# Performance work log

Measured on AMD Instinct MI355X. Metric: run time of the kernel, lower is better.

## Reference

```python
import jax, jax.numpy as jnp
import numpy as np

H, NH, NKV, HD, S, B = 4096, 32, 8, 128, 2048, 1
QMAX = 127.0  # int8 symmetric


def fake_quant(x, axis=None):
    """Symmetric int8 fake quantization with straight-through estimator.
    axis=None -> per-tensor dynamic scale; axis=int -> per-channel along that axis."""
    if axis is None:
        amax = jnp.max(jnp.abs(x))
    else:
        amax = jnp.max(jnp.abs(x), axis=axis, keepdims=True)
    scale = jnp.maximum(amax, 1e-8) / QMAX
    q = jnp.clip(jnp.round(x / scale), -QMAX - 1, QMAX) * scale
    return x + jax.lax.stop_gradient(q - x)


def quant_linear(x, w):
    # weight: per-output-channel quant (reduce over in-features axis=1);
    # activation: per-tensor dynamic quant
    xq = fake_quant(x)
    wq = fake_quant(w, axis=1)
    return jnp.einsum('bsh,oh->bso', xq, wq)


def rotate_half(x):
    x1, x2 = jnp.split(x, 2, axis=-1)
    return jnp.concatenate([-x2, x1], axis=-1)


def apply_rope(q, k, cos, sin):
    # q: [B,NH,S,HD], k: [B,NKV,S,HD], cos/sin: [B,S,HD]
    cos = cos[:, None, :, :]
    sin = sin[:, None, :, :]
    return q * cos + rotate_half(q) * sin, k * cos + rotate_half(k) * sin


def setup_inputs() -> dict:
    key = jax.random.key(0)
    ks = jax.random.split(key, 6)
    hidden_states = jax.random.normal(ks[0], (B, S, H), jnp.float32)
    # additive causal mask
    neg = jnp.finfo(jnp.float32).min
    mask = jnp.where(jnp.tril(jnp.ones((S, S), bool)), 0.0, neg)
    attention_mask = jnp.broadcast_to(mask, (B, 1, S, S)).astype(jnp.float32)
    # rotary cos/sin
    inv_freq = 1.0 / (10000.0 ** (jnp.arange(0, HD, 2, dtype=jnp.float32) / HD))
    t = jnp.arange(S, dtype=jnp.float32)
    freqs = jnp.outer(t, inv_freq)                     # [S, HD/2]
    emb = jnp.concatenate([freqs, freqs], axis=-1)     # [S, HD]
    cos = jnp.broadcast_to(jnp.cos(emb), (B, S, HD))
    sin = jnp.broadcast_to(jnp.sin(emb), (B, S, HD))
    sc = 0.02
    wq = jax.random.normal(ks[1], (H, H), jnp.float32) * sc
    wk = jax.random.normal(ks[2], (NKV * HD, H), jnp.float32) * sc
    wv = jax.random.normal(ks[3], (NKV * HD, H), jnp.float32) * sc
    wo = jax.random.normal(ks[4], (H, H), jnp.float32) * sc
    return {"hidden_states": hidden_states, "attention_mask": attention_mask,
            "cos": cos, "sin": sin, "wq": wq, "wk": wk, "wv": wv, "wo": wo}


def reference(hidden_states, attention_mask, cos, sin, wq, wk, wv, wo):
    b, s, _ = hidden_states.shape
    scaling = HD ** -0.5
    q = quant_linear(hidden_states, wq).reshape(b, s, NH, HD).transpose(0, 2, 1, 3)
    k = quant_linear(hidden_states, wk).reshape(b, s, NKV, HD).transpose(0, 2, 1, 3)
    v = quant_linear(hidden_states, wv).reshape(b, s, NKV, HD).transpose(0, 2, 1, 3)
    q, k = apply_rope(q, k, cos, sin)
    groups = NH // NKV
    k = jnp.repeat(k, groups, axis=1)  # [B,NH,S,HD]
    v = jnp.repeat(v, groups, axis=1)
    # quantize before QK^T
    qq = fake_quant(q)
    kq = fake_quant(k)
    attn = jnp.einsum('bhqd,bhkd->bhqk', qq, kq) * scaling
    attn = attn + attention_mask
    attn = jnp.maximum(attn, jnp.finfo(attn.dtype).min)
    attn = jax.nn.softmax(attn.astype(jnp.float32), axis=-1).astype(q.dtype)
    # quantize before PV
    pq = fake_quant(attn)
    vq = fake_quant(v)
    out = jnp.einsum('bhqk,bhkd->bhqd', pq, vq)
    out = out.transpose(0, 2, 1, 3).reshape(b, s, NH * HD)
    out = quant_linear(out, wo)
    return out
```

## Files before the change

### kernel.cpp

```cpp
#include <hip/hip_runtime.h>
#include <cstdint>
#include <cstddef>


#define S_LEN   2048
#define HDIM    4096
#define NHEADS  32
#define NKVH    8
#define HEADD   128
#define QMAXF   127.0f
#define ROPE_BLOCKS 20480

typedef _Float16 half8  __attribute__((ext_vector_type(8)));
typedef float    floatx4 __attribute__((ext_vector_type(4)));

__device__ __forceinline__ float wave_max64(float v){
#pragma unroll
  for (int off = 32; off > 0; off >>= 1) v = fmaxf(v, __shfl_xor(v, off));
  return v;
}
__device__ __forceinline__ float grp16_max(float v){
#pragma unroll
  for (int off = 8; off > 0; off >>= 1) v = fmaxf(v, __shfl_xor(v, off));
  return v;
}
__device__ __forceinline__ float grp16_sum(float v){
#pragma unroll
  for (int off = 8; off > 0; off >>= 1) v += __shfl_xor(v, off);
  return v;
}
__device__ __forceinline__ void atomic_max_f(unsigned* p, float v){
  atomicMax(p, __float_as_uint(v));
}
__device__ __forceinline__ float q8(float x, float scale){
  return fminf(fmaxf(rintf(x / scale), -128.f), 127.f);
}
__device__ __forceinline__ void gload_lds16(const _Float16* g, _Float16* l){
  __builtin_amdgcn_global_load_lds((const __attribute__((address_space(1))) void*)g,
                                   (__attribute__((address_space(3))) void*)l, 16, 0, 0);
}

__device__ __forceinline__ void block_atomic_max(float m, unsigned* out){
  m = wave_max64(m);
  __shared__ float red[4];
  int wid = threadIdx.x >> 6;
  if ((threadIdx.x & 63) == 0) red[wid] = m;
  __syncthreads();
  if (threadIdx.x == 0)
    atomic_max_f(out, fmaxf(fmaxf(red[0], red[1]), fmaxf(red[2], red[3])));
}

__global__ void k_init(float* scal){ if (threadIdx.x < 16) scal[threadIdx.x] = 0.0f; }

__global__ void k_amax(const float* __restrict__ x, size_t n4, unsigned* __restrict__ out){
  size_t i = (size_t)blockIdx.x * blockDim.x + threadIdx.x;
  size_t stride = (size_t)gridDim.x * blockDim.x;
  float m = 0.f;
  for (; i < n4; i += stride){
    float4 v = ((const float4*)x)[i];
    m = fmaxf(m, fmaxf(fmaxf(fabsf(v.x), fabsf(v.y)), fmaxf(fabsf(v.z), fabsf(v.w))));
  }
  block_atomic_max(m, out);
}

__global__ void k_amax_v(const float* __restrict__ Y, unsigned* __restrict__ out){
  size_t i = (size_t)blockIdx.x * blockDim.x + threadIdx.x;
  size_t stride = (size_t)gridDim.x * blockDim.x;
  float m = 0.f;
  for (size_t e = i; e < (size_t)S_LEN * 1024; e += stride){
    size_t s = e >> 10; int c = (int)(e & 1023);
    m = fmaxf(m, fabsf(Y[s * 6144 + 5120 + c]));
  }
  block_atomic_max(m, out);
}

__global__ void k_quant(const float* __restrict__ x, _Float16* __restrict__ q,
                        size_t n4, const float* __restrict__ amax){
  float scale = fmaxf(*amax, 1e-8f) / QMAXF;
  size_t i = (size_t)blockIdx.x * blockDim.x + threadIdx.x;
  size_t stride = (size_t)gridDim.x * blockDim.x;
  for (; i < n4; i += stride){
    float4 v = ((const float4*)x)[i];
    union { _Float16 h[4]; uint2 u; } pk;
    pk.h[0] = (_Float16)q8(v.x, scale);
    pk.h[1] = (_Float16)q8(v.y, scale);
    pk.h[2] = (_Float16)q8(v.z, scale);
    pk.h[3] = (_Float16)q8(v.w, scale);
    ((uint2*)q)[i] = pk.u;
  }
}

__global__ __launch_bounds__(256) void k_quant_w(
    const float* __restrict__ wq, const float* __restrict__ wk,
    const float* __restrict__ wv, const float* __restrict__ wo,
    _Float16* __restrict__ Wall, _Float16* __restrict__ Wo,
    float* __restrict__ wsc)
{
  int row = blockIdx.x;
  const float* src; _Float16* dst;
  if (row < 4096)      { src = wq + (size_t)row * HDIM;          dst = Wall + (size_t)row * HDIM; }
  else if (row < 5120) { src = wk + (size_t)(row - 4096) * HDIM; dst = Wall + (size_t)row * HDIM; }
  else if (row < 6144) { src = wv + (size_t)(row - 5120) * HDIM; dst = Wall + (size_t)row * HDIM; }
  else                 { src = wo + (size_t)(row - 6144) * HDIM; dst = Wo + (size_t)(row - 6144) * HDIM; }
  float4 v[4]; float m = 0.f;
#pragma unroll
  for (int i = 0; i < 4; i++){
    v[i] = ((const float4*)src)[threadIdx.x + i * 256];
    m = fmaxf(m, fmaxf(fmaxf(fabsf(v[i].x), fabsf(v[i].y)), fmaxf(fabsf(v[i].z), fabsf(v[i].w))));
  }
  m = wave_max64(m);
  __shared__ float red[4];
  int wid = threadIdx.x >> 6;
  if ((threadIdx.x & 63) == 0) red[wid] = m;
  __syncthreads();
  float am = fmaxf(fmaxf(red[0], red[1]), fmaxf(red[2], red[3]));
  float scale = fmaxf(am, 1e-8f) / QMAXF;
  if (threadIdx.x == 0) wsc[row] = scale;
#pragma unroll
  for (int i = 0; i < 4; i++){
    union { _Float16 h[4]; uint2 u; } pk;
    pk.h[0] = (_Float16)q8(v[i].x, scale);
    pk.h[1] = (_Float16)q8(v[i].y, scale);
    pk.h[2] = (_Float16)q8(v[i].z, scale);
    pk.h[3] = (_Float16)q8(v[i].w, scale);
    ((uint2*)dst)[threadIdx.x + i * 256] = pk.u;
  }
}

__global__ __launch_bounds__(256) void k_rope(
    float* __restrict__ Y, const float* __restrict__ cosb,
    const float* __restrict__ sinb,
    float* __restrict__ qpart, float* __restrict__ kpart)
{
  int idx = blockIdx.x * 256 + threadIdx.x;
  int s = idx / (40 * 64);
  int rem = idx - s * 40 * 64;
  int head = rem >> 6;
  int d = rem & 63;
  size_t base = (size_t)s * 6144 + (head < 32 ? head * 128 : 4096 + (head - 32) * 128);
  float x1 = Y[base + d], x2 = Y[base + d + 64];
  float c1 = cosb[s * 128 + d],      s1 = sinb[s * 128 + d];
  float c2 = cosb[s * 128 + d + 64], s2 = sinb[s * 128 + d + 64];
  float o1 = x1 * c1 - x2 * s1;
  float o2 = x2 * c2 + x1 * s2;
  Y[base + d] = o1; Y[base + d + 64] = o2;
  float m = wave_max64(fmaxf(fabsf(o1), fabsf(o2)));
  __shared__ float wmax[4]; __shared__ int wisq[4];
  int wid = threadIdx.x >> 6;
  if ((threadIdx.x & 63) == 0){ wmax[wid] = m; wisq[wid] = (head < 32); }
  __syncthreads();
  if (threadIdx.x == 0){
    float qm = 0.f, km = 0.f;
#pragma unroll
    for (int w = 0; w < 4; w++){
      if (wisq[w]) qm = fmaxf(qm, wmax[w]); else km = fmaxf(km, wmax[w]);
    }
    qpart[blockIdx.x] = qm; kpart[blockIdx.x] = km;
  }
}

__global__ __launch_bounds__(256) void k_reduce_qk(
    const float* __restrict__ qpart, const float* __restrict__ kpart,
    float* __restrict__ scal)
{
  const float* src = blockIdx.x ? kpart : qpart;
  float m = 0.f;
  for (int i = threadIdx.x; i < ROPE_BLOCKS; i += 256) m = fmaxf(m, src[i]);
  m = wave_max64(m);
  __shared__ float red[4];
  int wid = threadIdx.x >> 6;
  if ((threadIdx.x & 63) == 0) red[wid] = m;
  __syncthreads();
  if (threadIdx.x == 0)
    scal[1 + blockIdx.x] = fmaxf(fmaxf(red[0], red[1]), fmaxf(red[2], red[3]));
}

__global__ __launch_bounds__(256) void k_quant_qk(
    const float* __restrict__ Y, _Float16* __restrict__ Qh,
    _Float16* __restrict__ Kh, const float* __restrict__ scal)
{
  int i = blockIdx.x * 256 + threadIdx.x;
  int s = i / 1280, c4 = i - s * 1280;
  int col = c4 * 4;
  float4 v = *(const float4*)(Y + (size_t)s * 6144 + col);
  float scale = fmaxf(col < 4096 ? scal[1] : scal[2], 1e-8f) / QMAXF;
  union { _Float16 h[4]; uint2 u; } pk;
  pk.h[0] = (_Float16)q8(v.x, scale);
  pk.h[1] = (_Float16)q8(v.y, scale);
  pk.h[2] = (_Float16)q8(v.z, scale);
  pk.h[3] = (_Float16)q8(v.w, scale);
  if (col < 4096) *(uint2*)(Qh + (size_t)s * 4096 + col) = pk.u;
  else            *(uint2*)(Kh + (size_t)s * 1024 + (col - 4096)) = pk.u;
}

__global__ __launch_bounds__(256) void k_quant_vt(
    const float* __restrict__ Y, _Float16* __restrict__ Vt,
    const float* __restrict__ scal)
{
  __shared__ _Float16 sT[64][72];
  const int s0 = blockIdx.x * 64, kvh = blockIdx.y, dh = blockIdx.z;
  const float scale = fmaxf(scal[3], 1e-8f) / QMAXF;
  const int d = threadIdx.x & 63, srow = threadIdx.x >> 6;
#pragma unroll
  for (int i = 0; i < 16; i++){
    int s = srow + i * 4;
    float v = Y[(size_t)(s0 + s) * 6144 + 5120 + kvh * 128 + dh * 64 + d];
    sT[d][s] = (_Float16)q8(v, scale);
  }
  __syncthreads();
  const int dr = threadIdx.x >> 2, j = threadIdx.x & 3;
  _Float16* dst = Vt + (size_t)kvh * HEADD * S_LEN + (size_t)(dh * 64 + dr) * S_LEN + s0 + j * 16;
  *(uint4*)(dst)     = *(const uint4*)(&sT[dr][j * 16]);
  *(uint4*)(dst + 8) = *(const uint4*)(&sT[dr][j * 16 + 8]);
}

__global__ __launch_bounds__(256) void k_gemm_nt(
    const _Float16* __restrict__ A, const _Float16* __restrict__ B,
    const float* __restrict__ amax_a, const float* __restrict__ sb,
    float* __restrict__ C, int M, int N, int K)
{
  __shared__ _Float16 sA[128 * 32];
  __shared__ _Float16 sB[128 * 32];
  const int m0 = blockIdx.x * 128;
  const int n0 = blockIdx.y * 128;
  const int tid = threadIdx.x;
  const int w = tid >> 6, lane = tid & 63;
  const int quad = lane >> 4, l16 = lane & 15;
  const int wm = (w & 1) * 64, wn = (w >> 1) * 64;
  floatx4 acc[4][4] = {};
  const int srow = w * 16 + (lane >> 2);
  const int scol = (lane & 3) * 8;
  const _Float16* gA0 = A + (size_t)(m0 + srow) * K + scol;
  const _Float16* gA1 = A + (size_t)(m0 + 64 + srow) * K + scol;
  const _Float16* gB0 = B + (size_t)(n0 + srow) * K + scol;
  const _Float16* gB1 = B + (size_t)(n0 + 64 + srow) * K + scol;
  _Float16* dA0 = sA + w * 512 + lane * 8;
  _Float16* dA1 = sA + 2048 + w * 512 + lane * 8;
  _Float16* dB0 = sB + w * 512 + lane * 8;
  _Float16* dB1 = sB + 2048 + w * 512 + lane * 8;

  for (int k0 = 0; k0 < K; k0 += 32){
    __syncthreads();
    gload_lds16(gA0 + k0, dA0);
    gload_lds16(gA1 + k0, dA1);
    gload_lds16(gB0 + k0, dB0);
    gload_lds16(gB1 + k0, dB1);
    __syncthreads();
    half8 af[4], bf[4];
#pragma unroll
    for (int i = 0; i < 4; i++){
      af[i] = *(const half8*)(sA + (wm + i * 16 + l16) * 32 + quad * 8);
      bf[i] = *(const half8*)(sB + (wn + i * 16 + l16) * 32 + quad * 8);
    }
#pragma unroll
    for (int i = 0; i < 4; i++)
#pragma unroll
      for (int j = 0; j < 4; j++)
        acc[i][j] = __builtin_amdgcn_mfma_f32_16x16x32_f16(af[i], bf[j], acc[i][j], 0, 0, 0);
  }
  const float sa = fmaxf(*amax_a, 1e-8f) / QMAXF;
#pragma unroll
  for (int i = 0; i < 4; i++){
    int row = m0 + wm + i * 16 + quad * 4;
#pragma unroll
    for (int j = 0; j < 4; j++){
      int col = n0 + wn + j * 16 + l16;
      float sc2 = sa * sb[col];
#pragma unroll
      for (int rr = 0; rr < 4; rr++)
        C[(size_t)(row + rr) * N + col] = acc[i][j][rr] * sc2;
    }
  }
}

__global__ __launch_bounds__(256, 4) void k_attn(
    const _Float16* __restrict__ Qh,
    const _Float16* __restrict__ Kh,
    const _Float16* __restrict__ Vt,
    const float* __restrict__ scal,
    float* __restrict__ AO)
{
  const int jj = blockIdx.y >> 3;
  const int aa = (jj & 2) ? (int)((blockIdx.x + 16) & 31) : (int)blockIdx.x;
  const int qb = (jj & 1) ? (31 - aa) : aa;
  const int h   = blockIdx.y;
  const int kvh = h >> 2;
  const int tid = threadIdx.x;
  const int wid = tid >> 6, lane = tid & 63;
  const int quad = lane >> 4, l16 = lane & 15;

  __shared__ _Float16 sKV[2][8192];
  __shared__ _Float16 sP[4][1024];

  const float s_q = fmaxf(scal[1], 1e-8f) / QMAXF;
  const float s_k = fmaxf(scal[2], 1e-8f) / QMAXF;
  const float s_v = fmaxf(scal[3], 1e-8f) / QMAXF;
  const float qkscale = s_q * s_k * 0.08838834764831845f;
  const float osc = s_v * (1.0f / QMAXF);

  const int r   = tid >> 2, seg = tid & 3;
  int kst[4];
#pragma unroll
  for (int i = 0; i < 4; i++){
    int c = seg * 4 + i;
    kst[i] = r * 128 + ((c & 8) | ((c ^ (r & 7)) & 7)) * 8;
  }
  const int vr = tid >> 1, vh = tid & 1;
  int vst[4];
#pragma unroll
  for (int i = 0; i < 4; i++){
    int c = vh * 4 + i;
    vst[i] = vr * 64 + ((c ^ (vr & 7)) & 7) * 8;
  }
  int krd[4];
#pragma unroll
  for (int kk = 0; kk < 4; kk++){
    int c = kk * 4 + quad;
    krd[kk] = l16 * 128 + ((c & 8) | ((c ^ (l16 & 7)) & 7)) * 8;
  }
  const int vrd0 = l16 * 64 + ((quad       ^ (l16 & 7)) & 7) * 8;
  const int vrd1 = l16 * 64 + (((quad ^ 4) ^ (l16 & 7)) & 7) * 8;

  const _Float16* gK0 = Kh + (size_t)r * 1024 + (size_t)kvh * 128 + seg * 32;
  const _Float16* gV0 = Vt + (size_t)kvh * (HEADD * S_LEN) + (size_t)vr * S_LEN + vh * 32;

  const int qrow = qb * 64 + wid * 16 + l16;
  half8 qf[4];
#pragma unroll
  for (int kk = 0; kk < 4; kk++)
    qf[kk] = *(const half8*)(Qh + (size_t)qrow * 4096 + h * 128 + kk * 32 + quad * 8);
  const int q_of_reg = qb * 64 + wid * 16 + quad * 4;

  float mrow[4], lrow[4];
#pragma unroll
  for (int rr = 0; rr < 4; rr++){ mrow[rr] = -__builtin_inff(); lrow[rr] = 0.f; }

  {
    const uint4* g = (const uint4*)gK0;
    uint4 t0 = g[0], t1 = g[1], t2 = g[2], t3 = g[3];
    _Float16* b = sKV[0];
    *(uint4*)(b + kst[0]) = t0; *(uint4*)(b + kst[1]) = t1;
    *(uint4*)(b + kst[2]) = t2; *(uint4*)(b + kst[3]) = t3;
  }
  __syncthreads();

  for (int kt = 0; kt <= qb; ++kt){
    uint4 t0, t1, t2, t3;
    if (kt < qb){
      const uint4* g = (const uint4*)(gK0 + (size_t)(kt + 1) * 65536);
      t0 = g[0]; t1 = g[1]; t2 = g[2]; t3 = g[3];
    }
    const _Float16* kb = sKV[kt & 1];
    float sv[4][4];
    const bool diag = (kt == qb);
    __builtin_amdgcn_s_setprio(1);
#pragma unroll
    for (int nt = 0; nt < 4; nt++){
      floatx4 c = {};
#pragma unroll
      for (int kk = 0; kk < 4; kk++){
        half8 bf = *(const half8*)(kb + nt * 2048 + krd[kk]);
        c = __builtin_amdgcn_mfma_f32_16x16x32_f16(qf[kk], bf, c, 0, 0, 0);
      }
      if (diag){
        int kpos = kt * 64 + nt * 16 + l16;
#pragma unroll
        for (int rr = 0; rr < 4; rr++)
          sv[nt][rr] = (kpos <= q_of_reg + rr) ? c[rr] * qkscale : -__builtin_inff();
      } else {
#pragma unroll
        for (int rr = 0; rr < 4; rr++) sv[nt][rr] = c[rr] * qkscale;
      }
    }
    __builtin_amdgcn_s_setprio(0);
    if (kt < qb){
      _Float16* b = sKV[(kt + 1) & 1];
      *(uint4*)(b + kst[0]) = t0; *(uint4*)(b + kst[1]) = t1;
      *(uint4*)(b + kst[2]) = t2; *(uint4*)(b + kst[3]) = t3;
    }
#pragma unroll
    for (int rr = 0; rr < 4; rr++){
      float lmax = fmaxf(fmaxf(sv[0][rr], sv[1][rr]), fmaxf(sv[2][rr], sv[3][rr]));
      float tmax = grp16_max(lmax);
      float mnew = fmaxf(mrow[rr], tmax);
      float lsum = 0.f;
#pragma unroll
      for (int nt = 0; nt < 4; nt++) lsum += __expf(sv[nt][rr] - mnew);
      lsum = grp16_sum(lsum);
      lrow[rr] = lrow[rr] * __expf(mrow[rr] - mnew) + lsum;
      mrow[rr] = mnew;
    }
    __syncthreads();
  }

  float il[4];
#pragma unroll
  for (int rr = 0; rr < 4; rr++) il[rr] = QMAXF * __builtin_amdgcn_rcpf(lrow[rr]);

  floatx4 accO[8] = {};
  _Float16* sKb = sKV[0];
  _Float16* sVb = sKV[1];
  _Float16* sPw = sP[wid];

  uint4 t0, t1, t2, t3, u0, u1, u2, u3;
  {
    const uint4* g  = (const uint4*)gK0;
    t0 = g[0];  t1 = g[1];  t2 = g[2];  t3 = g[3];
    const uint4* gv = (const uint4*)gV0;
    u0 = gv[0]; u1 = gv[1]; u2 = gv[2]; u3 = gv[3];
  }
  for (int kt = 0; kt <= qb; ++kt){
    __syncthreads();
    *(uint4*)(sKb + kst[0]) = t0; *(uint4*)(sKb + kst[1]) = t1;
    *(uint4*)(sKb + kst[2]) = t2; *(uint4*)(sKb + kst[3]) = t3;
    *(uint4*)(sVb + vst[0]) = u0; *(uint4*)(sVb + vst[1]) = u1;
    *(uint4*)(sVb + vst[2]) = u2; *(uint4*)(sVb + vst[3]) = u3;
    __syncthreads();
    const bool diag = (kt == qb);
    __builtin_amdgcn_s_setprio(1);
#pragma unroll
    for (int nt = 0; nt < 4; nt++){
      floatx4 c = {};
#pragma unroll
      for (int kk = 0; kk < 4; kk++){
        half8 bf = *(const half8*)(sKb + nt * 2048 + krd[kk]);
        c = __builtin_amdgcn_mfma_f32_16x16x32_f16(qf[kk], bf, c, 0, 0, 0);
      }
      int kpos = kt * 64 + nt * 16 + l16;
#pragma unroll
      for (int rr = 0; rr < 4; rr++){
        float pq = fminf(rintf(__expf(c[rr] * qkscale - mrow[rr]) * il[rr]), 127.f);
        if (diag && kpos > q_of_reg + rr) pq = 0.f;
        int row = quad * 4 + rr;
        sPw[row * 64 + ((nt * 2 + (l16 >> 3)) ^ (row & 7)) * 8 + (l16 & 7)] = (_Float16)pq;
      }
    }
    __builtin_amdgcn_s_setprio(0);
    if (kt < qb){
      const uint4* g  = (const uint4*)(gK0 + (size_t)(kt + 1) * 65536);
      t0 = g[0];  t1 = g[1];  t2 = g[2];  t3 = g[3];
      const uint4* gv = (const uint4*)(gV0 + (size_t)(kt + 1) * 64);
      u0 = gv[0]; u1 = gv[1]; u2 = gv[2]; u3 = gv[3];
    }
    half8 pf0 = *(const half8*)(sPw + vrd0);
    half8 pf1 = *(const half8*)(sPw + vrd1);
    __builtin_amdgcn_s_setprio(1);
#pragma unroll
    for (int dt = 0; dt < 8; dt++){
      half8 b0 = *(const half8*)(sVb + dt * 1024 + vrd0);
      half8 b1 = *(const half8*)(sVb + dt * 1024 + vrd1);
      accO[dt] = __builtin_amdgcn_mfma_f32_16x16x32_f16(pf0, b0, accO[dt], 0, 0, 0);
      accO[dt] = __builtin_amdgcn_mfma_f32_16x16x32_f16(pf1, b1, accO[dt], 0, 0, 0);
    }
    __builtin_amdgcn_s_setprio(0);
  }

#pragma unroll
  for (int dt = 0; dt < 8; dt++){
    int col = h * 128 + dt * 16 + l16;
#pragma unroll
    for (int rr = 0; rr < 4; rr++)
      AO[(size_t)(q_of_reg + rr) * 4096 + col] = accO[dt][rr] * osc;
  }
}

extern "C" void kernel_launch(void* const* d_in, const int* in_sizes, int n_in,
                              void* d_out, int out_size, void* d_ws, size_t ws_size,
                              hipStream_t stream)
{
  const float* hidden = (const float*)d_in[0];
  const float* cosb = (const float*)d_in[2];
  const float* sinb = (const float*)d_in[3];
  const float* wq = (const float*)d_in[4];
  const float* wk = (const float*)d_in[5];
  const float* wv = (const float*)d_in[6];
  const float* wo = (const float*)d_in[7];
  float* out = (float*)d_out;

  char* ws = (char*)d_ws;
  size_t off = 0;
  auto alloc = [&](size_t bytes){ size_t o = off; off += (bytes + 255) & ~(size_t)255; return o; };
  float*    scal  = (float*)   (ws + alloc(64));
  float*    wsc   = (float*)   (ws + alloc(10240 * 4));
  float*    qpart = (float*)   (ws + alloc(ROPE_BLOCKS * 4));
  float*    kpart = (float*)   (ws + alloc(ROPE_BLOCKS * 4));
  _Float16* Wall  = (_Float16*)(ws + alloc((size_t)6144 * 4096 * 2));
  _Float16* Wo    = (_Float16*)(ws + alloc((size_t)4096 * 4096 * 2));
  _Float16* Xq    = (_Float16*)(ws + alloc((size_t)2048 * 4096 * 2));
  float*    Y     = (float*)   (ws + alloc((size_t)2048 * 6144 * 4));
  _Float16* Qh  = Xq;
  _Float16* Kh  = Wall;
  _Float16* Vt  = Wall + (size_t)2048 * 1024;
  float*    AO  = Y;
  _Float16* AOq = (_Float16*)((char*)Y + (size_t)2048 * 4096 * 4);

  unsigned* su = (unsigned*)scal;

  k_init<<<dim3(1), dim3(64), 0, stream>>>(scal);
  k_quant_w<<<dim3(10240), dim3(256), 0, stream>>>(wq, wk, wv, wo, Wall, Wo, wsc);
  k_amax<<<dim3(256), dim3(256), 0, stream>>>(hidden, (size_t)(2048 * 4096 / 4), su + 0);
  k_quant<<<dim3(2048), dim3(256), 0, stream>>>(hidden, Xq, (size_t)(2048 * 4096 / 4), scal + 0);
  k_gemm_nt<<<dim3(16, 48), dim3(256), 0, stream>>>(Xq, Wall, scal + 0, wsc, Y, 2048, 6144, 4096);
  k_rope<<<dim3(ROPE_BLOCKS), dim3(256), 0, stream>>>(Y, cosb, sinb, qpart, kpart);
  k_reduce_qk<<<dim3(2), dim3(256), 0, stream>>>(qpart, kpart, scal);
  k_amax_v<<<dim3(256), dim3(256), 0, stream>>>(Y, su + 3);
  k_quant_qk<<<dim3(10240), dim3(256), 0, stream>>>(Y, Qh, Kh, scal);
  k_quant_vt<<<dim3(32, 8, 2), dim3(256), 0, stream>>>(Y, Vt, scal);
  k_attn<<<dim3(32, 32), dim3(256), 0, stream>>>(Qh, Kh, Vt, scal, AO);
  k_amax<<<dim3(256), dim3(256), 0, stream>>>(AO, (size_t)(2048 * 4096 / 4), su + 4);
  k_quant<<<dim3(2048), dim3(256), 0, stream>>>(AO, AOq, (size_t)(2048 * 4096 / 4), scal + 4);
  k_gemm_nt<<<dim3(16, 32), dim3(256), 0, stream>>>(AOq, Wo, scal + 4, wsc + 6144, out, 2048, 4096, 4096);
}
```

Before: 735.5 us.

## Stage attention K/V tiles with direct global-to-LDS loads instead of registers

The attention kernel now copies K and V tiles straight from global memory into LDS through a direct-load helper, in place of loading into registers and then storing to LDS. The XOR swizzle is moved onto the global source addresses so the LDS layout stays the same. This saves registers and LDS store instructions. In the second pass, however, the loads are now issued right before the barrier, so they no longer overlap with the previous tile's compute. The launch-bounds occupancy hint is also lowered from 4 to 2 blocks per CU.

```diff
diff --git a/kernel.cpp b/kernel.cpp
--- a/kernel.cpp
+++ b/kernel.cpp
@@ -273,7 +273,7 @@
   }
 }
 
-__global__ __launch_bounds__(256, 4) void k_attn(
+__global__ __launch_bounds__(256, 2) void k_attn(
     const _Float16* __restrict__ Qh,
     const _Float16* __restrict__ Kh,
     const _Float16* __restrict__ Vt,
@@ -298,20 +298,13 @@
   const float qkscale = s_q * s_k * 0.08838834764831845f;
   const float osc = s_v * (1.0f / QMAXF);
 
-  const int r   = tid >> 2, seg = tid & 3;
-  int kst[4];
-#pragma unroll
-  for (int i = 0; i < 4; i++){
-    int c = seg * 4 + i;
-    kst[i] = r * 128 + ((c & 8) | ((c ^ (r & 7)) & 7)) * 8;
-  }
-  const int vr = tid >> 1, vh = tid & 1;
-  int vst[4];
-#pragma unroll
-  for (int i = 0; i < 4; i++){
-    int c = vh * 4 + i;
-    vst[i] = vr * 64 + ((c ^ (vr & 7)) & 7) * 8;
-  }
+  const int srow7 = (wid * 4 + quad) & 7;
+  const int sch   = (l16 & 8) | ((l16 ^ srow7) & 7);
+  const _Float16* gKs = Kh + (size_t)(wid * 4 + quad) * 1024 + (size_t)kvh * 128 + sch * 8;
+  const int vrg = lane >> 3, vp = lane & 7;
+  const _Float16* gVs = Vt + (size_t)kvh * (HEADD * S_LEN)
+                           + (size_t)(wid * 8 + vrg) * S_LEN + ((vp ^ vrg) & 7) * 8;
+
   int krd[4];
 #pragma unroll
   for (int kk = 0; kk < 4; kk++){
@@ -321,9 +314,6 @@
   const int vrd0 = l16 * 64 + ((quad       ^ (l16 & 7)) & 7) * 8;
   const int vrd1 = l16 * 64 + (((quad ^ 4) ^ (l16 & 7)) & 7) * 8;
 
-  const _Float16* gK0 = Kh + (size_t)r * 1024 + (size_t)kvh * 128 + seg * 32;
-  const _Float16* gV0 = Vt + (size_t)kvh * (HEADD * S_LEN) + (size_t)vr * S_LEN + vh * 32;
-
   const int qrow = qb * 64 + wid * 16 + l16;
   half8 qf[4];
 #pragma unroll
@@ -335,21 +325,28 @@
 #pragma unroll
   for (int rr = 0; rr < 4; rr++){ mrow[rr] = -__builtin_inff(); lrow[rr] = 0.f; }
 
-  {
-    const uint4* g = (const uint4*)gK0;
-    uint4 t0 = g[0], t1 = g[1], t2 = g[2], t3 = g[3];
-    _Float16* b = sKV[0];
-    *(uint4*)(b + kst[0]) = t0; *(uint4*)(b + kst[1]) = t1;
-    *(uint4*)(b + kst[2]) = t2; *(uint4*)(b + kst[3]) = t3;
-  }
+  auto stage_k = [&](int kt, _Float16* buf){
+    const _Float16* g = gKs + (size_t)kt * 65536;
+    _Float16* d = buf + wid * 512;
+    gload_lds16(g,          d);
+    gload_lds16(g + 16384,  d + 2048);
+    gload_lds16(g + 32768,  d + 4096);
+    gload_lds16(g + 49152,  d + 6144);
+  };
+  auto stage_v = [&](int kt, _Float16* buf){
+    const _Float16* g = gVs + (size_t)kt * 64;
+    _Float16* d = buf + wid * 512;
+    gload_lds16(g,          d);
+    gload_lds16(g + 65536,  d + 2048);
+    gload_lds16(g + 131072, d + 4096);
+    gload_lds16(g + 196608, d + 6144);
+  };
+
+  stage_k(0, sKV[0]);
   __syncthreads();
 
   for (int kt = 0; kt <= qb; ++kt){
-    uint4 t0, t1, t2, t3;
-    if (kt < qb){
-      const uint4* g = (const uint4*)(gK0 + (size_t)(kt + 1) * 65536);
-      t0 = g[0]; t1 = g[1]; t2 = g[2]; t3 = g[3];
-    }
+    if (kt < qb) stage_k(kt + 1, sKV[(kt + 1) & 1]);
     const _Float16* kb = sKV[kt & 1];
     float sv[4][4];
     const bool diag = (kt == qb);
@@ -373,11 +370,6 @@
       }
     }
     __builtin_amdgcn_s_setprio(0);
-    if (kt < qb){
-      _Float16* b = sKV[(kt + 1) & 1];
-      *(uint4*)(b + kst[0]) = t0; *(uint4*)(b + kst[1]) = t1;
-      *(uint4*)(b + kst[2]) = t2; *(uint4*)(b + kst[3]) = t3;
-    }
 #pragma unroll
     for (int rr = 0; rr < 4; rr++){
       float lmax = fmaxf(fmaxf(sv[0][rr], sv[1][rr]), fmaxf(sv[2][rr], sv[3][rr]));
@@ -402,19 +394,10 @@
   _Float16* sVb = sKV[1];
   _Float16* sPw = sP[wid];
 
-  uint4 t0, t1, t2, t3, u0, u1, u2, u3;
-  {
-    const uint4* g  = (const uint4*)gK0;
-    t0 = g[0];  t1 = g[1];  t2 = g[2];  t3 = g[3];
-    const uint4* gv = (const uint4*)gV0;
-    u0 = gv[0]; u1 = gv[1]; u2 = gv[2]; u3 = gv[3];
-  }
   for (int kt = 0; kt <= qb; ++kt){
     __syncthreads();
-    *(uint4*)(sKb + kst[0]) = t0; *(uint4*)(sKb + kst[1]) = t1;
-    *(uint4*)(sKb + kst[2]) = t2; *(uint4*)(sKb + kst[3]) = t3;
-    *(uint4*)(sVb + vst[0]) = u0; *(uint4*)(sVb + vst[1]) = u1;
-    *(uint4*)(sVb + vst[2]) = u2; *(uint4*)(sVb + vst[3]) = u3;
+    stage_k(kt, sKb);
+    stage_v(kt, sVb);
     __syncthreads();
     const bool diag = (kt == qb);
     __builtin_amdgcn_s_setprio(1);
@@ -436,12 +419,6 @@
       }
     }
     __builtin_amdgcn_s_setprio(0);
-    if (kt < qb){
-      const uint4* g  = (const uint4*)(gK0 + (size_t)(kt + 1) * 65536);
-      t0 = g[0];  t1 = g[1];  t2 = g[2];  t3 = g[3];
-      const uint4* gv = (const uint4*)(gV0 + (size_t)(kt + 1) * 64);
-      u0 = gv[0]; u1 = gv[1]; u2 = gv[2]; u3 = gv[3];
-    }
     half8 pf0 = *(const half8*)(sPw + vrd0);
     half8 pf1 = *(const half8*)(sPw + vrd1);
     __builtin_amdgcn_s_setprio(1);
```

Measured after the change: 679.9 us. 7.6% less time.
